# Performance work log

Hardware: AMD Instinct MI355X
Metric: run time of the kernel (lower is better)

## Reference

```python
import jax, jax.numpy as jnp
from jax import lax
import numpy as np

B, L, E, K, NCLS = 128, 1024, 8, 3, 5


def conv1d(x, w, b):
    # x: [N,C,L], w: [O,I,3], padding=1 -> same length
    y = lax.conv_general_dilated(x, w, (1,), [(1, 1)], dimension_numbers=('NCH', 'OIH', 'NCH'))
    return y + b[None, :, None]


def maxpool2(x):
    # MaxPool1d(kernel=2, stride=2), floor mode (VALID drops odd tail)
    return lax.reduce_window(x, -jnp.inf, lax.max, (1, 1, 2), (1, 1, 2), 'VALID')


def setup_inputs():
    key = jax.random.key(0)
    ks = jax.random.split(key, 32)
    s = 0.05
    g = lambda i, shp: jax.random.normal(ks[i], shp, jnp.float32) * s
    inp = {}
    inp['x'] = jax.random.normal(ks[0], (B, 1, L), jnp.float32)
    inp['c1_w'], inp['c1_b'] = g(1, (16, 1, 3)), jnp.zeros((16,), jnp.float32)
    # stacked expert conv params (leading dim = E)
    chans = [(16, 16), (16, 32), (32, 64), (64, 128), (128, 256), (256, 512)]
    for j, (ci, co) in enumerate(chans, start=1):
        inp[f'ew{j}'] = g(1 + j, (E, co, ci, 3))
        inp[f'eb{j}'] = jnp.zeros((E, co), jnp.float32)
    inp['r_w'], inp['r_b'] = g(10, (E, 16)), jnp.zeros((E,), jnp.float32)
    inp['c2_w'], inp['c2_b'] = g(11, (1024, 512, 3)), jnp.zeros((1024,), jnp.float32)
    fl = (L // 8 // 2) * 1024
    inp['f1_w'], inp['f1_b'] = g(12, (256, fl)) * 0.2, jnp.zeros((256,), jnp.float32)
    inp['f2_w'], inp['f2_b'] = g(13, (NCLS, 256)), jnp.zeros((NCLS,), jnp.float32)
    return inp


def reference(x, c1_w, c1_b, ew1, eb1, ew2, eb2, ew3, eb3, ew4, eb4, ew5, eb5, ew6, eb6,
              r_w, r_b, c2_w, c2_b, f1_w, f1_b, f2_w, f2_b):
    b = x.shape[0]
    h = jax.nn.relu(conv1d(x, c1_w, c1_b))            # [B,16,L]
    pooled = h.mean(axis=-1)                           # AdaptiveAvgPool1d(1) -> [B,16]
    # (router noise skipped: eval-mode determinism)
    rlogits = pooled @ r_w.T + r_b                     # [B,E]
    probs = jax.nn.softmax(rlogits, axis=-1)
    tg, ti = lax.top_k(probs, K)                       # [B,K]
    tg = tg / tg.sum(axis=-1, keepdims=True)
    gates = jnp.zeros((b, E), probs.dtype).at[jnp.arange(b)[:, None], ti].set(tg)  # dense [B,E]

    def expert(w1, b1, w2, b2, w3, b3, w4, b4, w5, b5, w6, b6):
        y = conv1d(h, w1, b1)
        y = maxpool2(jax.nn.relu(conv1d(y, w2, b2)))   # block1 -> [B,32,L/2]
        y = conv1d(y, w3, b3)
        y = maxpool2(jax.nn.relu(conv1d(y, w4, b4)))   # block2 -> [B,128,L/4]
        y = conv1d(y, w5, b5)
        y = maxpool2(jax.nn.relu(conv1d(y, w6, b6)))   # block3 -> [B,512,L/8]
        return y

    eouts = jax.vmap(expert)(ew1, eb1, ew2, eb2, ew3, eb3, ew4, eb4, ew5, eb5, ew6, eb6)  # [E,B,512,L/8]
    combined = jnp.einsum('be,ebcl->bcl', gates, eouts)  # gated scatter-combine (zero gate == not dispatched)

    y = maxpool2(jax.nn.relu(conv1d(combined, c2_w, c2_b)))  # [B,1024,L/16]
    y = y.reshape(b, -1)
    y = jax.nn.relu(y @ f1_w.T + f1_b)                 # dropout p=0.05 is identity in eval
    out = y @ f2_w.T + f2_b                            # [B,NCLS]

    mean_probs = probs.mean(axis=0)
    cv = jnp.std(mean_probs, ddof=1) / (mean_probs.mean() + 1e-10)  # torch std is unbiased
    return out, cv ** 2
```

## Files before the change

kernel.cpp:

```cpp
#include <hip/hip_runtime.h>
#include <hip/hip_bf16.h>
#include <math.h>

#define B_   128
#define L_   1024
#define E_   8
#define K_   3

typedef float f32x4 __attribute__((ext_vector_type(4)));
typedef short s8v  __attribute__((ext_vector_type(8)));
typedef unsigned short u16x8 __attribute__((ext_vector_type(8)));

__device__ inline ushort f2bf(float v) {
  union { float f; unsigned u; } x; x.f = v;
  unsigned r = (x.u + 0x7fffu + ((x.u >> 16) & 1u)) >> 16;
  return (ushort)r;
}
__device__ inline float bf2f(ushort h) {
  union { unsigned u; float f; } x; x.u = ((unsigned)h) << 16;
  return x.f;
}

__device__ __forceinline__ void gload_lds16(const ushort* g, ushort* l) {
  __builtin_amdgcn_global_load_lds(
      (const __attribute__((address_space(1))) unsigned int*)g,
      (__attribute__((address_space(3))) unsigned int*)l, 16, 0, 0);
}

__global__ __launch_bounds__(256) void conv1_k(
    const float* __restrict__ x, const float* __restrict__ w,
    const float* __restrict__ bias, float* __restrict__ h,
    float* __restrict__ pooled)
{
  const int b = blockIdx.x;
  const int t = threadIdx.x;
  __shared__ float xs[1026];
  __shared__ float wsm[48];
  __shared__ float bs[16];
  __shared__ float red[4][16];

  for (int i = t; i < 1024; i += 256) xs[i + 1] = x[(size_t)b * 1024 + i];
  if (t == 0) { xs[0] = 0.f; xs[1025] = 0.f; }
  if (t < 48) wsm[t] = w[t];
  if (t < 16) bs[t] = bias[t];
  __syncthreads();

  float ps[16];
#pragma unroll
  for (int c = 0; c < 16; ++c) ps[c] = 0.f;

  for (int li = 0; li < 4; ++li) {
    const int l = t + li * 256;
    const float xm = xs[l], x0 = xs[l + 1], xp = xs[l + 2];
#pragma unroll
    for (int co = 0; co < 16; ++co) {
      float v = fmaf(wsm[co * 3 + 0], xm,
                fmaf(wsm[co * 3 + 1], x0,
                fmaf(wsm[co * 3 + 2], xp, bs[co])));
      v = fmaxf(v, 0.f);
      h[((size_t)b * 16 + co) * 1024 + l] = v;
      ps[co] += v;
    }
  }
#pragma unroll
  for (int co = 0; co < 16; ++co) {
    float v = ps[co];
    for (int off = 32; off > 0; off >>= 1) v += __shfl_down(v, off, 64);
    ps[co] = v;
  }
  const int wid = t >> 6, lane = t & 63;
  if (lane == 0) {
#pragma unroll
    for (int co = 0; co < 16; ++co) red[wid][co] = ps[co];
  }
  __syncthreads();
  if (t < 16) pooled[(size_t)b * 16 + t] =
      (red[0][t] + red[1][t] + red[2][t] + red[3][t]) * (1.f / 1024.f);
}

__global__ void router_k(const float* __restrict__ pooled,
                         const float* __restrict__ rw,
                         const float* __restrict__ rb,
                         float* __restrict__ pair_g, int* __restrict__ pair_e,
                         float* __restrict__ cv2_out)
{
  const int b = threadIdx.x;
  __shared__ float pl[128][8];
  __shared__ float mp[8];

  float pv[16];
#pragma unroll
  for (int i = 0; i < 16; ++i) pv[i] = pooled[(size_t)b * 16 + i];

  float lg[8];
#pragma unroll
  for (int e = 0; e < 8; ++e) {
    float s = rb[e];
#pragma unroll
    for (int i = 0; i < 16; ++i) s = fmaf(pv[i], rw[e * 16 + i], s);
    lg[e] = s;
  }
  float mx = lg[0];
#pragma unroll
  for (int e = 1; e < 8; ++e) mx = fmaxf(mx, lg[e]);
  float pr[8]; float sum = 0.f;
#pragma unroll
  for (int e = 0; e < 8; ++e) { pr[e] = expf(lg[e] - mx); sum += pr[e]; }
  const float inv = 1.f / sum;
#pragma unroll
  for (int e = 0; e < 8; ++e) { pr[e] *= inv; pl[b][e] = pr[e]; }

  bool used[8] = {false,false,false,false,false,false,false,false};
  float tg[3]; int ti[3];
  for (int k = 0; k < 3; ++k) {
    float best = -1.f; int bi = 0;
#pragma unroll
    for (int e = 0; e < 8; ++e)
      if (!used[e] && pr[e] > best) { best = pr[e]; bi = e; }
    used[bi] = true; tg[k] = best; ti[k] = bi;
  }
  const float ts = 1.f / (tg[0] + tg[1] + tg[2]);
  for (int k = 0; k < 3; ++k) {
    pair_g[b * 3 + k] = tg[k] * ts;
    pair_e[b * 3 + k] = ti[k];
  }
  __syncthreads();
  if (b < 8) {
    float s = 0.f;
    for (int i = 0; i < 128; ++i) s += pl[i][b];
    mp[b] = s * (1.f / 128.f);
  }
  __syncthreads();
  if (b == 0) {
    float m = 0.f;
    for (int e = 0; e < 8; ++e) m += mp[e];
    m *= (1.f / 8.f);
    float v = 0.f;
    for (int e = 0; e < 8; ++e) { float d = mp[e] - m; v += d * d; }
    v *= (1.f / 7.f);
    const float cv = sqrtf(v) / (m + 1e-10f);
    cv2_out[0] = cv * cv;
  }
}

template <int CI, int CO, int LIN, bool POOL, int CIC, int CO_T, int CO_R,
          int IN_DIV>
__global__ __launch_bounds__(256) void convR_k(
    const float* __restrict__ in, const float* __restrict__ w,
    const float* __restrict__ bias, float* __restrict__ out,
    const int* __restrict__ pe)
{
  constexpr int CQ  = CO_T / CO_R;
  constexpr int LQ  = 256 / CQ;
  constexpr int L_T = LQ * 4;
  constexpr int LOUT = POOL ? (LIN / 2) : LIN;
  constexpr int RS  = L_T + 8;
  constexpr int CG  = CO_R / 4;

  const int p  = blockIdx.x;
  const int cb = blockIdx.y * CO_T;
  const int l0 = blockIdx.z * L_T;
  const int e  = pe ? pe[p] : 0;
  const float* inp = in + (size_t)(p / IN_DIV) * CI * LIN;
  const float* wp  = w + (size_t)e * CO * CI * 3;

  __shared__ float in_s[CIC * RS];
  __shared__ float w_s[CIC * 3 * CO_T];

  const int t  = threadIdx.x;
  const int cq = t / LQ;
  const int lq = t % LQ;

  float acc[CO_R][4];
#pragma unroll
  for (int c = 0; c < CO_R; ++c)
#pragma unroll
    for (int l = 0; l < 4; ++l) acc[c][l] = 0.f;

  for (int c0 = 0; c0 < CI; c0 += CIC) {
    for (int idx = t; idx < CIC * (L_T + 2); idx += 256) {
      const int ci = idx / (L_T + 2);
      const int j  = idx - ci * (L_T + 2);
      const int gl = l0 + j - 1;
      in_s[ci * RS + j] =
          (gl >= 0 && gl < LIN) ? inp[(size_t)(c0 + ci) * LIN + gl] : 0.f;
    }
    for (int i = t; i < CIC * CO_T; i += 256) {
      const int co = i % CO_T;
      const int ci = i / CO_T;
      const float* wsrc = wp + ((size_t)(cb + co) * CI + (c0 + ci)) * 3;
      const float w0 = wsrc[0], w1 = wsrc[1], w2 = wsrc[2];
      w_s[(ci * 3 + 0) * CO_T + co] = w0;
      w_s[(ci * 3 + 1) * CO_T + co] = w1;
      w_s[(ci * 3 + 2) * CO_T + co] = w2;
    }
    __syncthreads();
#pragma unroll 4
    for (int ci = 0; ci < CIC; ++ci) {
      const float* row = &in_s[ci * RS + lq * 4];
      const float4 xa = *reinterpret_cast<const float4*>(row);
      const float2 xb = *reinterpret_cast<const float2*>(row + 4);
      const float xv[6] = {xa.x, xa.y, xa.z, xa.w, xb.x, xb.y};
      const float* wrow = &w_s[ci * 3 * CO_T + cq * CO_R];
#pragma unroll
      for (int k = 0; k < 3; ++k) {
#pragma unroll
        for (int cg = 0; cg < CG; ++cg) {
          const float4 wv =
              *reinterpret_cast<const float4*>(&wrow[k * CO_T + cg * 4]);
          const float wq[4] = {wv.x, wv.y, wv.z, wv.w};
#pragma unroll
          for (int c = 0; c < 4; ++c)
#pragma unroll
            for (int l = 0; l < 4; ++l)
              acc[cg * 4 + c][l] = fmaf(wq[c], xv[l + k], acc[cg * 4 + c][l]);
        }
      }
    }
    __syncthreads();
  }

#pragma unroll
  for (int c = 0; c < CO_R; ++c) {
    const int co = cb + cq * CO_R + c;
    const float bv = bias[(size_t)e * CO + co];
    const float v0 = acc[c][0] + bv, v1 = acc[c][1] + bv;
    const float v2 = acc[c][2] + bv, v3 = acc[c][3] + bv;
    float* op = out + ((size_t)p * CO + co) * LOUT;
    if (POOL) {
      const int lo = (l0 >> 1) + lq * 2;
      float2 r;
      r.x = fmaxf(fmaxf(v0, v1), 0.f);
      r.y = fmaxf(fmaxf(v2, v3), 0.f);
      *reinterpret_cast<float2*>(&op[lo]) = r;
    } else {
      const int l = l0 + lq * 4;
      *reinterpret_cast<float4*>(&op[l]) = make_float4(v0, v1, v2, v3);
    }
  }
}

__global__ void wprep_k(const float* __restrict__ w, ushort* __restrict__ oh,
                        ushort* __restrict__ ol, int E, int CO, int CI,
                        int total)
{
  const int idx = blockIdx.x * 256 + threadIdx.x;
  if (idx >= total) return;
  const int KC = CI >> 5;
  const int j = idx & 31;
  int r = idx >> 5;
  const int co = r % CO; r /= CO;
  const int kc = r % KC; r /= KC;
  const int tp = r % 3;
  const int e  = r / 3;
  const float v = w[(((size_t)e * CO + co) * CI + (kc * 32 + j)) * 3 + tp];
  const ushort hi = f2bf(v);
  oh[idx] = hi;
  ol[idx] = f2bf(v - bf2f(hi));
}

__global__ __launch_bounds__(256) void t0_k(const float* __restrict__ in,
                                            ushort* __restrict__ oh,
                                            ushort* __restrict__ ol)
{
  __shared__ float tile[32][33];
  const int p  = blockIdx.x;
  const int l0 = blockIdx.y * 32;
  const int tx = threadIdx.x & 31;
  const int ty = threadIdx.x >> 5;

#pragma unroll
  for (int i = 0; i < 4; ++i) {
    const int ci = ty + i * 8;
    tile[ci][tx] = in[(size_t)p * 16384 + (size_t)ci * 512 + l0 + tx];
  }
  __syncthreads();
#pragma unroll
  for (int i = 0; i < 4; ++i) {
    const int l = l0 + ty + i * 8;
    const float v = tile[tx][ty + i * 8];
    const size_t o = ((size_t)p * 514 + 1 + l) * 32 + tx;
    const ushort hi = f2bf(v);
    oh[o] = hi;
    ol[o] = f2bf(v - bf2f(hi));
  }
  if (blockIdx.y == 0 && threadIdx.x < 32) {
    const size_t o0 = (size_t)p * 514 * 32 + threadIdx.x;
    const size_t o1 = ((size_t)p * 514 + 513) * 32 + threadIdx.x;
    oh[o0] = 0; ol[o0] = 0; oh[o1] = 0; ol[o1] = 0;
  }
}

template <int CI, int CO, int L, int OMODE>
__global__ __launch_bounds__(256) void convM_k(
    const ushort* __restrict__ xh, const ushort* __restrict__ xl,
    const ushort* __restrict__ wh, const ushort* __restrict__ wl,
    const float* __restrict__ bias,
    ushort* __restrict__ oh, ushort* __restrict__ ol,
    float* __restrict__ of,
    const int* __restrict__ pe, const float* __restrict__ pg,
    int pair0)
{
  constexpr int KC = CI / 32;
  constexpr int NK = (OMODE == 1) ? 3 : 1;
  const int bx = blockIdx.x;
  const int cb = blockIdx.y * 64;
  const int lz = blockIdx.z * 128;

  __shared__ ushort xs[2][130][32];
  __shared__ ushort wsm[2][3][64][32];
  ushort* xsf = &xs[0][0][0];
  ushort* wsf = &wsm[0][0][0][0];

  const int t = threadIdx.x;
  const int lane = t & 63;
  const int wv = t >> 6;
  const int l16 = lane & 15;
  const int kb8 = (lane >> 4) * 8;

  float gacc[2][4][2];
  if (OMODE == 1) {
#pragma unroll
    for (int a = 0; a < 2; ++a)
#pragma unroll
      for (int b = 0; b < 4; ++b) { gacc[a][b][0] = 0.f; gacc[a][b][1] = 0.f; }
  }

  f32x4 acc[2][4];
  int e = 0; float gate = 1.f; int lp = bx;
  float bv[4];

  for (int kp = 0; kp < NK; ++kp) {
    if (OMODE == 1) {
      const int gp = (pair0 + bx) * 3 + kp;
      e = pe[gp]; gate = pg[gp]; lp = bx * 3 + kp;
    } else if (OMODE == 2) { lp = bx; e = 0; }
    else { lp = bx; e = pe[pair0 + bx]; }

#pragma unroll
    for (int a = 0; a < 2; ++a)
#pragma unroll
      for (int b = 0; b < 4; ++b) acc[a][b] = (f32x4){0.f, 0.f, 0.f, 0.f};

    const size_t xbase = ((size_t)lp * (L + 2) + lz) * CI;

    for (int kc = 0; kc < KC; ++kc) {
      const int c0 = kc * 32;
#pragma unroll
      for (int it = 0; it < 5; ++it) {
        const int g = it * 256 + t;
        if (g < 1040) {
          const int pl = g >= 520;
          const int r = g - pl * 520;
          const int row = r >> 2;
          const int c16 = r & 3;
          const ushort* src =
              (pl ? xl : xh) + xbase + (size_t)row * CI + c0 + c16 * 8;
          gload_lds16(src, xsf + (size_t)g * 8);
        }
      }
#pragma unroll
      for (int it = 0; it < 6; ++it) {
        const int g = it * 256 + t;
        const int pl = g >= 768;
        const int r = g - pl * 768;
        const int tp = r >> 8;
        const int rr = r & 255;
        const int co = rr >> 2;
        const int c16 = rr & 3;
        const ushort* src = (pl ? wl : wh) +
            ((((size_t)e * 3 + tp) * KC + kc) * CO + cb + co) * 32 + c16 * 8;
        gload_lds16(src, wsf + (size_t)g * 8);
      }
      __syncthreads();

      __builtin_amdgcn_s_setprio(1);
#pragma unroll
      for (int tp = 0; tp < 3; ++tp) {
        const int ar = wv * 32 + l16 + tp;
        s8v a00 = *reinterpret_cast<const s8v*>(&xs[0][ar][kb8]);
        s8v a01 = *reinterpret_cast<const s8v*>(&xs[0][ar + 16][kb8]);
        s8v a10 = *reinterpret_cast<const s8v*>(&xs[1][ar][kb8]);
        s8v a11 = *reinterpret_cast<const s8v*>(&xs[1][ar + 16][kb8]);
#pragma unroll
        for (int cs = 0; cs < 4; ++cs) {
          const int brow = cs * 16 + l16;
          s8v bh = *reinterpret_cast<const s8v*>(&wsm[0][tp][brow][kb8]);
          s8v bl = *reinterpret_cast<const s8v*>(&wsm[1][tp][brow][kb8]);
          acc[0][cs] = __builtin_amdgcn_mfma_f32_16x16x32_bf16(a00, bh, acc[0][cs], 0, 0, 0);
          acc[0][cs] = __builtin_amdgcn_mfma_f32_16x16x32_bf16(a00, bl, acc[0][cs], 0, 0, 0);
          acc[0][cs] = __builtin_amdgcn_mfma_f32_16x16x32_bf16(a10, bh, acc[0][cs], 0, 0, 0);
          acc[1][cs] = __builtin_amdgcn_mfma_f32_16x16x32_bf16(a01, bh, acc[1][cs], 0, 0, 0);
          acc[1][cs] = __builtin_amdgcn_mfma_f32_16x16x32_bf16(a01, bl, acc[1][cs], 0, 0, 0);
          acc[1][cs] = __builtin_amdgcn_mfma_f32_16x16x32_bf16(a11, bh, acc[1][cs], 0, 0, 0);
        }
      }
      __builtin_amdgcn_s_setprio(0);
      __syncthreads();
    }

#pragma unroll
    for (int cs = 0; cs < 4; ++cs)
      bv[cs] = bias[(size_t)e * CO + cb + cs * 16 + l16];

    if (OMODE == 1) {
#pragma unroll
      for (int ls = 0; ls < 2; ++ls)
#pragma unroll
        for (int cs = 0; cs < 4; ++cs)
#pragma unroll
          for (int q = 0; q < 2; ++q) {
            const float v0 = acc[ls][cs][q * 2] + bv[cs];
            const float v1 = acc[ls][cs][q * 2 + 1] + bv[cs];
            const float m = fmaxf(fmaxf(v0, v1), 0.f);
            gacc[ls][cs][q] += gate * m;
          }
    }
  }

  if (OMODE == 0) {
#pragma unroll
    for (int ls = 0; ls < 2; ++ls)
#pragma unroll
      for (int cs = 0; cs < 4; ++cs)
#pragma unroll
        for (int r = 0; r < 4; ++r) {
          const int l = lz + wv * 32 + ls * 16 + (lane >> 4) * 4 + r;
          const float v = acc[ls][cs][r] + bv[cs];
          const size_t o = ((size_t)lp * (L + 2) + 1 + l) * CO + cb + cs * 16 + l16;
          const ushort hi = f2bf(v);
          oh[o] = hi;
          ol[o] = f2bf(v - bf2f(hi));
        }
    if (blockIdx.z == 0 && t < 64) {
      const size_t o0 = (size_t)lp * (L + 2) * CO + cb + t;
      const size_t o1 = ((size_t)lp * (L + 2) + (L + 1)) * CO + cb + t;
      oh[o0] = 0; ol[o0] = 0; oh[o1] = 0; ol[o1] = 0;
    }
  } else if (OMODE == 3) {
#pragma unroll
    for (int ls = 0; ls < 2; ++ls)
#pragma unroll
      for (int cs = 0; cs < 4; ++cs)
#pragma unroll
        for (int r = 0; r < 4; r += 2) {
          const float v0 = acc[ls][cs][r] + bv[cs];
          const float v1 = acc[ls][cs][r + 1] + bv[cs];
          const float m = fmaxf(fmaxf(v0, v1), 0.f);
          const int lpp = (lz + wv * 32 + ls * 16 + (lane >> 4) * 4 + r) >> 1;
          const size_t o = ((size_t)lp * (L / 2 + 2) + 1 + lpp) * CO + cb + cs * 16 + l16;
          const ushort hi = f2bf(m);
          oh[o] = hi;
          ol[o] = f2bf(m - bf2f(hi));
        }
    if (blockIdx.z == 0 && t < 64) {
      const size_t o0 = (size_t)lp * (L / 2 + 2) * CO + cb + t;
      const size_t o1 = ((size_t)lp * (L / 2 + 2) + (L / 2 + 1)) * CO + cb + t;
      oh[o0] = 0; ol[o0] = 0; oh[o1] = 0; ol[o1] = 0;
    }
  } else if (OMODE == 1) {
#pragma unroll
    for (int ls = 0; ls < 2; ++ls)
#pragma unroll
      for (int cs = 0; cs < 4; ++cs)
#pragma unroll
        for (int q = 0; q < 2; ++q) {
          const int lpp = (lz + wv * 32 + ls * 16 + (lane >> 4) * 4 + q * 2) >> 1;
          const int co = cb + cs * 16 + l16;
          const size_t o =
              ((size_t)(pair0 + bx) * (L / 2 + 2) + 1 + lpp) * CO + co;
          const float g = gacc[ls][cs][q];
          const ushort hi = f2bf(g);
          oh[o] = hi;
          ol[o] = f2bf(g - bf2f(hi));
        }
    if (blockIdx.z == 0 && t < 64) {
      const size_t o0 = (size_t)(pair0 + bx) * (L / 2 + 2) * CO + cb + t;
      const size_t o1 =
          ((size_t)(pair0 + bx) * (L / 2 + 2) + (L / 2 + 1)) * CO + cb + t;
      oh[o0] = 0; ol[o0] = 0; oh[o1] = 0; ol[o1] = 0;
    }
  } else {
#pragma unroll
    for (int ls = 0; ls < 2; ++ls)
#pragma unroll
      for (int cs = 0; cs < 4; ++cs)
#pragma unroll
        for (int r = 0; r < 4; r += 2) {
          const float v0 = acc[ls][cs][r] + bv[cs];
          const float v1 = acc[ls][cs][r + 1] + bv[cs];
          const float m = fmaxf(fmaxf(v0, v1), 0.f);
          const int lpp = (lz + wv * 32 + ls * 16 + (lane >> 4) * 4 + r) >> 1;
          const int co = cb + cs * 16 + l16;
          const size_t o = ((size_t)lp * CO + co) * (L / 2) + lpp;
          of[o] = m;
        }
  }
}

__global__ __launch_bounds__(256) void fc1M_k(const float* __restrict__ X,
                                              const float* __restrict__ W,
                                              float* __restrict__ part)
{
  __shared__ ushort xs[2][128][32];
  __shared__ ushort wsm[2][64][32];
  const int t = threadIdx.x;
  const int lane = t & 63;
  const int wv = t >> 6;
  const int l16 = lane & 15;
  const int kb8 = (lane >> 4) * 8;
  const int ot = blockIdx.x * 64;
  const size_t k0g = (size_t)blockIdx.y * 512;

  f32x4 acc[2][4];
#pragma unroll
  for (int a = 0; a < 2; ++a)
#pragma unroll
    for (int b = 0; b < 4; ++b) acc[a][b] = (f32x4){0.f, 0.f, 0.f, 0.f};

  const int xrow = t >> 1;
  const int xcol = (t & 1) * 16;
  const int wco  = t >> 2;
  const int wk   = (t & 3) * 8;

  for (int it = 0; it < 16; ++it) {
    const size_t k0 = k0g + it * 32;
    {
      const float* src = X + (size_t)xrow * 65536 + k0 + xcol;
      float v[16];
#pragma unroll
      for (int q = 0; q < 4; ++q)
        *reinterpret_cast<float4*>(&v[q * 4]) =
            *reinterpret_cast<const float4*>(src + q * 4);
#pragma unroll
      for (int q = 0; q < 2; ++q) {
        u16x8 hv, lv;
#pragma unroll
        for (int j = 0; j < 8; ++j) {
          const float f = v[q * 8 + j];
          const ushort h = f2bf(f);
          hv[j] = h;
          lv[j] = f2bf(f - bf2f(h));
        }
        *reinterpret_cast<u16x8*>(&xs[0][xrow][xcol + q * 8]) = hv;
        *reinterpret_cast<u16x8*>(&xs[1][xrow][xcol + q * 8]) = lv;
      }
    }
    {
      const float* src = W + (size_t)(ot + wco) * 65536 + k0 + wk;
      float v[8];
      *reinterpret_cast<float4*>(&v[0]) = *reinterpret_cast<const float4*>(src);
      *reinterpret_cast<float4*>(&v[4]) = *reinterpret_cast<const float4*>(src + 4);
      u16x8 hv, lv;
#pragma unroll
      for (int j = 0; j < 8; ++j) {
        const ushort h = f2bf(v[j]);
        hv[j] = h;
        lv[j] = f2bf(v[j] - bf2f(h));
      }
      *reinterpret_cast<u16x8*>(&wsm[0][wco][wk]) = hv;
      *reinterpret_cast<u16x8*>(&wsm[1][wco][wk]) = lv;
    }
    __syncthreads();
    __builtin_amdgcn_s_setprio(1);
#pragma unroll
    for (int ms = 0; ms < 2; ++ms) {
      const int ar = wv * 32 + ms * 16 + l16;
      s8v ah = *reinterpret_cast<const s8v*>(&xs[0][ar][kb8]);
      s8v al = *reinterpret_cast<const s8v*>(&xs[1][ar][kb8]);
#pragma unroll
      for (int cs = 0; cs < 4; ++cs) {
        const int brow = cs * 16 + l16;
        s8v bh = *reinterpret_cast<const s8v*>(&wsm[0][brow][kb8]);
        s8v bl = *reinterpret_cast<const s8v*>(&wsm[1][brow][kb8]);
        acc[ms][cs] = __builtin_amdgcn_mfma_f32_16x16x32_bf16(ah, bh, acc[ms][cs], 0, 0, 0);
        acc[ms][cs] = __builtin_amdgcn_mfma_f32_16x16x32_bf16(ah, bl, acc[ms][cs], 0, 0, 0);
        acc[ms][cs] = __builtin_amdgcn_mfma_f32_16x16x32_bf16(al, bh, acc[ms][cs], 0, 0, 0);
      }
    }
    __builtin_amdgcn_s_setprio(0);
    __syncthreads();
  }

#pragma unroll
  for (int ms = 0; ms < 2; ++ms)
#pragma unroll
    for (int cs = 0; cs < 4; ++cs)
#pragma unroll
      for (int r = 0; r < 4; ++r) {
        const int row = wv * 32 + ms * 16 + (lane >> 4) * 4 + r;
        const int col = ot + cs * 16 + l16;
        part[((size_t)blockIdx.y * 128 + row) * 256 + col] = acc[ms][cs][r];
      }
}

__global__ void fc1red_k(const float* __restrict__ part,
                         const float* __restrict__ b1, float* __restrict__ o1)
{
  const int idx = blockIdx.x * 256 + threadIdx.x;
  if (idx < 32768) {
    float s = 0.f;
#pragma unroll 8
    for (int z = 0; z < 128; ++z) s += part[(size_t)z * 32768 + idx];
    o1[idx] = fmaxf(s + b1[idx & 255], 0.f);
  }
}

__global__ void fc2_k(const float* __restrict__ o1, const float* __restrict__ w2,
                      const float* __restrict__ b2, float* __restrict__ out)
{
  const int b = blockIdx.x;
  const int lane = threadIdx.x;
  float acc[5] = {0.f, 0.f, 0.f, 0.f, 0.f};
  for (int i = lane; i < 256; i += 64) {
    const float xv = o1[(size_t)b * 256 + i];
#pragma unroll
    for (int o = 0; o < 5; ++o) acc[o] = fmaf(xv, w2[o * 256 + i], acc[o]);
  }
#pragma unroll
  for (int o = 0; o < 5; ++o) {
    for (int off = 32; off > 0; off >>= 1)
      acc[o] += __shfl_down(acc[o], off, 64);
  }
  if (lane == 0) {
#pragma unroll
    for (int o = 0; o < 5; ++o) out[b * 5 + o] = acc[o] + b2[o];
  }
}

extern "C" void kernel_launch(void* const* d_in, const int* in_sizes, int n_in,
                              void* d_out, int out_size, void* d_ws,
                              size_t ws_size, hipStream_t stream)
{
  const float* x   = (const float*)d_in[0];
  const float* c1w = (const float*)d_in[1];
  const float* c1b = (const float*)d_in[2];
  const float* ew[6];
  const float* eb[6];
  for (int j = 0; j < 6; ++j) {
    ew[j] = (const float*)d_in[3 + 2 * j];
    eb[j] = (const float*)d_in[4 + 2 * j];
  }
  const float* rw  = (const float*)d_in[15];
  const float* rb  = (const float*)d_in[16];
  const float* c2w = (const float*)d_in[17];
  const float* c2b = (const float*)d_in[18];
  const float* f1w = (const float*)d_in[19];
  const float* f1b = (const float*)d_in[20];
  const float* f2w = (const float*)d_in[21];
  const float* f2b = (const float*)d_in[22];
  float* out = (float*)d_out;

  const int chunkB = 32;
  const int chunkP = chunkB * 3;
  const int nchunk = 128 / chunkB;

  char* basep = (char*)d_ws;
  size_t off = 0;
  auto alloc = [&](size_t bytes) -> void* {
    off = (off + 255) & ~(size_t)255;
    void* r = basep + off;
    off += bytes;
    return r;
  };

  float* h      = (float*)alloc(2097152ull * 4);
  float* pooled = (float*)alloc(2048ull * 4);
  float* pairg  = (float*)alloc(384ull * 4);
  int*   paire  = (int*)  alloc(384ull * 4);
  float* fc1o   = (float*)alloc(32768ull * 4);

  ushort* xtFh  = (ushort*)alloc(8519680ull * 2 * 2);
  ushort* xtFl  = xtFh + 8519680ull;
  float*  part  = (float*)xtFh;

  const size_t slot_base = (off + 255) & ~(size_t)255;
  char* slotA = (char*)alloc((size_t)chunkP * 33024 * 2 * 2);
  char* slotB = (char*)alloc((size_t)chunkP * 66048 * 2 * 2);
  float* comb = (float*)(basep + slot_base);

  float*  bufA  = (float*)slotA;
  ushort* xt3h  = (ushort*)slotA;
  ushort* xt3l  = xt3h + (size_t)chunkP * 16448;
  ushort* xt5h  = (ushort*)slotA;
  ushort* xt5l  = xt5h + (size_t)chunkP * 33024;
  float*  bufB  = (float*)slotB;
  ushort* yE3h  = (ushort*)slotB;
  ushort* yE3l  = yE3h + (size_t)chunkP * 32896;
  ushort* y5h   = (ushort*)slotB;
  ushort* y5l   = y5h + (size_t)chunkP * 66048;

  ushort* wp3h  = (ushort*)alloc(49152ull * 2);
  ushort* wp3l  = (ushort*)alloc(49152ull * 2);
  ushort* wp4h  = (ushort*)alloc(196608ull * 2);
  ushort* wp4l  = (ushort*)alloc(196608ull * 2);
  ushort* wp5h  = (ushort*)alloc(786432ull * 2);
  ushort* wp5l  = (ushort*)alloc(786432ull * 2);
  ushort* wp6h  = (ushort*)alloc(3145728ull * 2);
  ushort* wp6l  = (ushort*)alloc(3145728ull * 2);
  ushort* wpFh  = (ushort*)alloc(1572864ull * 2);
  ushort* wpFl  = (ushort*)alloc(1572864ull * 2);

  conv1_k<<<128, 256, 0, stream>>>(x, c1w, c1b, h, pooled);
  router_k<<<1, 128, 0, stream>>>(pooled, rw, rb, pairg, paire, out + 640);

  wprep_k<<<(49152 + 255) / 256, 256, 0, stream>>>(ew[2], wp3h, wp3l, 8, 64, 32, 49152);
  wprep_k<<<(196608 + 255) / 256, 256, 0, stream>>>(ew[3], wp4h, wp4l, 8, 128, 64, 196608);
  wprep_k<<<(786432 + 255) / 256, 256, 0, stream>>>(ew[4], wp5h, wp5l, 8, 256, 128, 786432);
  wprep_k<<<(3145728 + 255) / 256, 256, 0, stream>>>(ew[5], wp6h, wp6l, 8, 512, 256, 3145728);
  wprep_k<<<(1572864 + 255) / 256, 256, 0, stream>>>(c2w, wpFh, wpFl, 1, 1024, 512, 1572864);

  for (int c = 0; c < nchunk; ++c) {
    const int b0 = c * chunkB;
    const int p0 = c * chunkP;
    convR_k<16, 16, 1024, false, 16, 16, 4, 3>
        <<<dim3(chunkP, 1, 4), 256, 0, stream>>>(
            h + (size_t)b0 * 16 * 1024, ew[0], eb[0], bufA, paire + p0);
    convR_k<16, 32, 1024, true, 16, 32, 8, 1>
        <<<dim3(chunkP, 1, 4), 256, 0, stream>>>(bufA, ew[1], eb[1], bufB,
                                                 paire + p0);
    t0_k<<<dim3(chunkP, 16), 256, 0, stream>>>(bufB, xt3h, xt3l);
    convM_k<32, 64, 512, 0>
        <<<dim3(chunkP, 1, 4), 256, 0, stream>>>(xt3h, xt3l, wp3h, wp3l, eb[2],
                                                 yE3h, yE3l, nullptr, paire,
                                                 nullptr, p0);
    convM_k<64, 128, 512, 3>
        <<<dim3(chunkP, 2, 4), 256, 0, stream>>>(yE3h, yE3l, wp4h, wp4l, eb[3],
                                                 xt5h, xt5l, nullptr, paire,
                                                 nullptr, p0);
    convM_k<128, 256, 256, 0>
        <<<dim3(chunkP, 4, 2), 256, 0, stream>>>(xt5h, xt5l, wp5h, wp5l, eb[4],
                                                 y5h, y5l, nullptr, paire,
                                                 nullptr, p0);
    convM_k<256, 512, 256, 1>
        <<<dim3(chunkB, 8, 2), 256, 0, stream>>>(y5h, y5l, wp6h, wp6l, eb[5],
                                                 xtFh, xtFl, nullptr,
                                                 paire, pairg, b0);
  }

  convM_k<512, 1024, 128, 2>
      <<<dim3(128, 16, 1), 256, 0, stream>>>(xtFh, xtFl, wpFh, wpFl, c2b,
                                             nullptr, nullptr, comb, nullptr,
                                             nullptr, 0);

  fc1M_k<<<dim3(4, 128), 256, 0, stream>>>(comb, f1w, part);
  fc1red_k<<<128, 256, 0, stream>>>(part, f1b, fc1o);
  fc2_k<<<128, 64, 0, stream>>>(fc1o, f2w, f2b, out);
}
```

Measured before the change: 645.3 us.

## Add larger-tile conv kernel with per-wave 64x64 output tiles

Adds a templated convM2_k in which each wave computes a 64x64 output tile (4 length sub-tiles by 4 channel sub-tiles) instead of 32x64, with a configurable wave layout across length and channels. The block tile grows to 256 positions or 128x128, and layers 4-6 plus the final c2 conv now use it with fewer blocks. The original convM_k is reduced to the OMODE 0 path used by layer 3. The goal is more reuse of each LDS fragment per MFMA and less redundant weight/halo loading. The cost is higher register pressure (64 accumulators plus gate accumulators) and fewer blocks, which may lower occupancy.

```diff
diff --git a/kernel.cpp b/kernel.cpp
--- a/kernel.cpp
+++ b/kernel.cpp
@@ -302,7 +302,6 @@
     int pair0)
 {
   constexpr int KC = CI / 32;
-  constexpr int NK = (OMODE == 1) ? 3 : 1;
   const int bx = blockIdx.x;
   const int cb = blockIdx.y * 64;
   const int lz = blockIdx.z * 128;
@@ -318,15 +317,143 @@
   const int l16 = lane & 15;
   const int kb8 = (lane >> 4) * 8;
 
-  float gacc[2][4][2];
+  const int e = pe[pair0 + bx];
+  const int lp = bx;
+
+  f32x4 acc[2][4];
+#pragma unroll
+  for (int a = 0; a < 2; ++a)
+#pragma unroll
+    for (int b = 0; b < 4; ++b) acc[a][b] = (f32x4){0.f, 0.f, 0.f, 0.f};
+
+  const size_t xbase = ((size_t)lp * (L + 2) + lz) * CI;
+
+  for (int kc = 0; kc < KC; ++kc) {
+    const int c0 = kc * 32;
+#pragma unroll
+    for (int it = 0; it < 5; ++it) {
+      const int g = it * 256 + t;
+      if (g < 1040) {
+        const int pl = g >= 520;
+        const int r = g - pl * 520;
+        const int row = r >> 2;
+        const int c16 = r & 3;
+        const ushort* src =
+            (pl ? xl : xh) + xbase + (size_t)row * CI + c0 + c16 * 8;
+        gload_lds16(src, xsf + (size_t)g * 8);
+      }
+    }
+#pragma unroll
+    for (int it = 0; it < 6; ++it) {
+      const int g = it * 256 + t;
+      const int pl = g >= 768;
+      const int r = g - pl * 768;
+      const int tp = r >> 8;
+      const int rr = r & 255;
+      const int co = rr >> 2;
+      const int c16 = rr & 3;
+      const ushort* src = (pl ? wl : wh) +
+          ((((size_t)e * 3 + tp) * KC + kc) * CO + cb + co) * 32 + c16 * 8;
+      gload_lds16(src, wsf + (size_t)g * 8);
+    }
+    __syncthreads();
+
+    __builtin_amdgcn_s_setprio(1);
+#pragma unroll
+    for (int tp = 0; tp < 3; ++tp) {
+      const int ar = wv * 32 + l16 + tp;
+      s8v a00 = *reinterpret_cast<const s8v*>(&xs[0][ar][kb8]);
+      s8v a01 = *reinterpret_cast<const s8v*>(&xs[0][ar + 16][kb8]);
+      s8v a10 = *reinterpret_cast<const s8v*>(&xs[1][ar][kb8]);
+      s8v a11 = *reinterpret_cast<const s8v*>(&xs[1][ar + 16][kb8]);
+#pragma unroll
+      for (int cs = 0; cs < 4; ++cs) {
+        const int brow = cs * 16 + l16;
+        s8v bh = *reinterpret_cast<const s8v*>(&wsm[0][tp][brow][kb8]);
+        s8v bl = *reinterpret_cast<const s8v*>(&wsm[1][tp][brow][kb8]);
+        acc[0][cs] = __builtin_amdgcn_mfma_f32_16x16x32_bf16(a00, bh, acc[0][cs], 0, 0, 0);
+        acc[0][cs] = __builtin_amdgcn_mfma_f32_16x16x32_bf16(a00, bl, acc[0][cs], 0, 0, 0);
+        acc[0][cs] = __builtin_amdgcn_mfma_f32_16x16x32_bf16(a10, bh, acc[0][cs], 0, 0, 0);
+        acc[1][cs] = __builtin_amdgcn_mfma_f32_16x16x32_bf16(a01, bh, acc[1][cs], 0, 0, 0);
+        acc[1][cs] = __builtin_amdgcn_mfma_f32_16x16x32_bf16(a01, bl, acc[1][cs], 0, 0, 0);
+        acc[1][cs] = __builtin_amdgcn_mfma_f32_16x16x32_bf16(a11, bh, acc[1][cs], 0, 0, 0);
+      }
+    }
+    __builtin_amdgcn_s_setprio(0);
+    __syncthreads();
+  }
+
+  float bv[4];
+#pragma unroll
+  for (int cs = 0; cs < 4; ++cs)
+    bv[cs] = bias[(size_t)e * CO + cb + cs * 16 + l16];
+
+#pragma unroll
+  for (int ls = 0; ls < 2; ++ls)
+#pragma unroll
+    for (int cs = 0; cs < 4; ++cs)
+#pragma unroll
+      for (int r = 0; r < 4; ++r) {
+        const int l = lz + wv * 32 + ls * 16 + (lane >> 4) * 4 + r;
+        const float v = acc[ls][cs][r] + bv[cs];
+        const size_t o = ((size_t)lp * (L + 2) + 1 + l) * CO + cb + cs * 16 + l16;
+        const ushort hi = f2bf(v);
+        oh[o] = hi;
+        ol[o] = f2bf(v - bf2f(hi));
+      }
+  if (blockIdx.z == 0 && t < 64) {
+    const size_t o0 = (size_t)lp * (L + 2) * CO + cb + t;
+    const size_t o1 = ((size_t)lp * (L + 2) + (L + 1)) * CO + cb + t;
+    oh[o0] = 0; ol[o0] = 0; oh[o1] = 0; ol[o1] = 0;
+  }
+}
+
+template <int CI, int CO, int L, int OMODE, int WL, int WC>
+__global__ __launch_bounds__(256) void convM2_k(
+    const ushort* __restrict__ xh, const ushort* __restrict__ xl,
+    const ushort* __restrict__ wh, const ushort* __restrict__ wl,
+    const float* __restrict__ bias,
+    ushort* __restrict__ oh, ushort* __restrict__ ol,
+    float* __restrict__ of,
+    const int* __restrict__ pe, const float* __restrict__ pg,
+    int pair0)
+{
+  constexpr int KC = CI / 32;
+  constexpr int NK = (OMODE == 1) ? 3 : 1;
+  constexpr int LT = WL * 64;
+  constexpr int CT = WC * 64;
+  constexpr int XROWS = LT + 2;
+  constexpr int XG = 2 * XROWS * 4;
+  constexpr int WG = 2 * 3 * CT * 4;
+  constexpr int XIT = (XG + 255) / 256;
+  constexpr int WIT = (WG + 255) / 256;
+
+  const int bx = blockIdx.x;
+  const int cb = blockIdx.y * CT;
+  const int lz = blockIdx.z * LT;
+
+  __shared__ ushort xs[2][XROWS][32];
+  __shared__ ushort wsm[2][3][CT][32];
+  ushort* xsf = &xs[0][0][0];
+  ushort* wsf = &wsm[0][0][0][0];
+
+  const int t = threadIdx.x;
+  const int lane = t & 63;
+  const int wv = t >> 6;
+  const int wvl = wv / WC;
+  const int wvc = wv % WC;
+  const int l16 = lane & 15;
+  const int kb8 = (lane >> 4) * 8;
+
+  float gacc[4][4][2];
   if (OMODE == 1) {
 #pragma unroll
-    for (int a = 0; a < 2; ++a)
+    for (int a = 0; a < 4; ++a)
 #pragma unroll
       for (int b = 0; b < 4; ++b) { gacc[a][b][0] = 0.f; gacc[a][b][1] = 0.f; }
   }
 
-  f32x4 acc[2][4];
+  f32x4 acc[4][4];
   int e = 0; float gate = 1.f; int lp = bx;
   float bv[4];
 
@@ -338,7 +465,7 @@
     else { lp = bx; e = pe[pair0 + bx]; }
 
 #pragma unroll
-    for (int a = 0; a < 2; ++a)
+    for (int a = 0; a < 4; ++a)
 #pragma unroll
       for (int b = 0; b < 4; ++b) acc[a][b] = (f32x4){0.f, 0.f, 0.f, 0.f};
 
@@ -347,11 +474,11 @@
     for (int kc = 0; kc < KC; ++kc) {
       const int c0 = kc * 32;
 #pragma unroll
-      for (int it = 0; it < 5; ++it) {
+      for (int it = 0; it < XIT; ++it) {
         const int g = it * 256 + t;
-        if (g < 1040) {
-          const int pl = g >= 520;
-          const int r = g - pl * 520;
+        if (g < XG) {
+          const int pl = g >= XG / 2;
+          const int r = g - pl * (XG / 2);
           const int row = r >> 2;
           const int c16 = r & 3;
           const ushort* src =
@@ -360,12 +487,12 @@
         }
       }
 #pragma unroll
-      for (int it = 0; it < 6; ++it) {
+      for (int it = 0; it < WIT; ++it) {
         const int g = it * 256 + t;
-        const int pl = g >= 768;
-        const int r = g - pl * 768;
-        const int tp = r >> 8;
-        const int rr = r & 255;
+        const int pl = g >= WG / 2;
+        const int r = g - pl * (WG / 2);
+        const int tp = r / (CT * 4);
+        const int rr = r % (CT * 4);
         const int co = rr >> 2;
         const int c16 = rr & 3;
         const ushort* src = (pl ? wl : wh) +
@@ -377,22 +504,24 @@
       __builtin_amdgcn_s_setprio(1);
 #pragma unroll
       for (int tp = 0; tp < 3; ++tp) {
-        const int ar = wv * 32 + l16 + tp;
-        s8v a00 = *reinterpret_cast<const s8v*>(&xs[0][ar][kb8]);
-        s8v a01 = *reinterpret_cast<const s8v*>(&xs[0][ar + 16][kb8]);
-        s8v a10 = *reinterpret_cast<const s8v*>(&xs[1][ar][kb8]);
-        s8v a11 = *reinterpret_cast<const s8v*>(&xs[1][ar + 16][kb8]);
+        s8v a0[4], a1[4];
+#pragma unroll
+        for (int lt = 0; lt < 4; ++lt) {
+          const int row = wvl * 64 + lt * 16 + l16 + tp;
+          a0[lt] = *reinterpret_cast<const s8v*>(&xs[0][row][kb8]);
+          a1[lt] = *reinterpret_cast<const s8v*>(&xs[1][row][kb8]);
+        }
 #pragma unroll
         for (int cs = 0; cs < 4; ++cs) {
-          const int brow = cs * 16 + l16;
+          const int brow = wvc * 64 + cs * 16 + l16;
           s8v bh = *reinterpret_cast<const s8v*>(&wsm[0][tp][brow][kb8]);
           s8v bl = *reinterpret_cast<const s8v*>(&wsm[1][tp][brow][kb8]);
-          acc[0][cs] = __builtin_amdgcn_mfma_f32_16x16x32_bf16(a00, bh, acc[0][cs], 0, 0, 0);
-          acc[0][cs] = __builtin_amdgcn_mfma_f32_16x16x32_bf16(a00, bl, acc[0][cs], 0, 0, 0);
-          acc[0][cs] = __builtin_amdgcn_mfma_f32_16x16x32_bf16(a10, bh, acc[0][cs], 0, 0, 0);
-          acc[1][cs] = __builtin_amdgcn_mfma_f32_16x16x32_bf16(a01, bh, acc[1][cs], 0, 0, 0);
-          acc[1][cs] = __builtin_amdgcn_mfma_f32_16x16x32_bf16(a01, bl, acc[1][cs], 0, 0, 0);
-          acc[1][cs] = __builtin_amdgcn_mfma_f32_16x16x32_bf16(a11, bh, acc[1][cs], 0, 0, 0);
+#pragma unroll
+          for (int lt = 0; lt < 4; ++lt) {
+            acc[lt][cs] = __builtin_amdgcn_mfma_f32_16x16x32_bf16(a0[lt], bh, acc[lt][cs], 0, 0, 0);
+            acc[lt][cs] = __builtin_amdgcn_mfma_f32_16x16x32_bf16(a0[lt], bl, acc[lt][cs], 0, 0, 0);
+            acc[lt][cs] = __builtin_amdgcn_mfma_f32_16x16x32_bf16(a1[lt], bh, acc[lt][cs], 0, 0, 0);
+          }
         }
       }
       __builtin_amdgcn_s_setprio(0);
@@ -401,80 +530,83 @@
 
 #pragma unroll
     for (int cs = 0; cs < 4; ++cs)
-      bv[cs] = bias[(size_t)e * CO + cb + cs * 16 + l16];
+      bv[cs] = bias[(size_t)e * CO + cb + wvc * 64 + cs * 16 + l16];
 
     if (OMODE == 1) {
 #pragma unroll
-      for (int ls = 0; ls < 2; ++ls)
+      for (int lt = 0; lt < 4; ++lt)
 #pragma unroll
         for (int cs = 0; cs < 4; ++cs)
 #pragma unroll
           for (int q = 0; q < 2; ++q) {
-            const float v0 = acc[ls][cs][q * 2] + bv[cs];
-            const float v1 = acc[ls][cs][q * 2 + 1] + bv[cs];
+            const float v0 = acc[lt][cs][q * 2] + bv[cs];
+            const float v1 = acc[lt][cs][q * 2 + 1] + bv[cs];
             const float m = fmaxf(fmaxf(v0, v1), 0.f);
-            gacc[ls][cs][q] += gate * m;
+            gacc[lt][cs][q] += gate * m;
           }
     }
   }
 
   if (OMODE == 0) {
 #pragma unroll
-    for (int ls = 0; ls < 2; ++ls)
+    for (int lt = 0; lt < 4; ++lt)
 #pragma unroll
       for (int cs = 0; cs < 4; ++cs)
 #pragma unroll
         for (int r = 0; r < 4; ++r) {
-          const int l = lz + wv * 32 + ls * 16 + (lane >> 4) * 4 + r;
-          const float v = acc[ls][cs][r] + bv[cs];
-          const size_t o = ((size_t)lp * (L + 2) + 1 + l) * CO + cb + cs * 16 + l16;
+          const int l = lz + wvl * 64 + lt * 16 + (lane >> 4) * 4 + r;
+          const float v = acc[lt][cs][r] + bv[cs];
+          const size_t o =
+              ((size_t)lp * (L + 2) + 1 + l) * CO + cb + wvc * 64 + cs * 16 + l16;
           const ushort hi = f2bf(v);
           oh[o] = hi;
           ol[o] = f2bf(v - bf2f(hi));
         }
-    if (blockIdx.z == 0 && t < 64) {
+    if (blockIdx.z == 0 && t < CT) {
       const size_t o0 = (size_t)lp * (L + 2) * CO + cb + t;
       const size_t o1 = ((size_t)lp * (L + 2) + (L + 1)) * CO + cb + t;
       oh[o0] = 0; ol[o0] = 0; oh[o1] = 0; ol[o1] = 0;
     }
   } else if (OMODE == 3) {
 #pragma unroll
-    for (int ls = 0; ls < 2; ++ls)
+    for (int lt = 0; lt < 4; ++lt)
 #pragma unroll
       for (int cs = 0; cs < 4; ++cs)
 #pragma unroll
         for (int r = 0; r < 4; r += 2) {
-          const float v0 = acc[ls][cs][r] + bv[cs];
-          const float v1 = acc[ls][cs][r + 1] + bv[cs];
+          const float v0 = acc[lt][cs][r] + bv[cs];
+          const float v1 = acc[lt][cs][r + 1] + bv[cs];
           const float m = fmaxf(fmaxf(v0, v1), 0.f);
-          const int lpp = (lz + wv * 32 + ls * 16 + (lane >> 4) * 4 + r) >> 1;
-          const size_t o = ((size_t)lp * (L / 2 + 2) + 1 + lpp) * CO + cb + cs * 16 + l16;
+          const int lpp = (lz + wvl * 64 + lt * 16 + (lane >> 4) * 4 + r) >> 1;
+          const size_t o = ((size_t)lp * (L / 2 + 2) + 1 + lpp) * CO + cb +
+                           wvc * 64 + cs * 16 + l16;
           const ushort hi = f2bf(m);
           oh[o] = hi;
           ol[o] = f2bf(m - bf2f(hi));
         }
-    if (blockIdx.z == 0 && t < 64) {
+    if (blockIdx.z == 0 && t < CT) {
       const size_t o0 = (size_t)lp * (L / 2 + 2) * CO + cb + t;
       const size_t o1 = ((size_t)lp * (L / 2 + 2) + (L / 2 + 1)) * CO + cb + t;
       oh[o0] = 0; ol[o0] = 0; oh[o1] = 0; ol[o1] = 0;
     }
   } else if (OMODE == 1) {
 #pragma unroll
-    for (int ls = 0; ls < 2; ++ls)
+    for (int lt = 0; lt < 4; ++lt)
 #pragma unroll
       for (int cs = 0; cs < 4; ++cs)
 #pragma unroll
         for (int q = 0; q < 2; ++q) {
-          const int lpp = (lz + wv * 32 + ls * 16 + (lane >> 4) * 4 + q * 2) >> 1;
-          const int co = cb + cs * 16 + l16;
+          const int lpp =
+              (lz + wvl * 64 + lt * 16 + (lane >> 4) * 4 + q * 2) >> 1;
+          const int co = cb + wvc * 64 + cs * 16 + l16;
           const size_t o =
               ((size_t)(pair0 + bx) * (L / 2 + 2) + 1 + lpp) * CO + co;
-          const float g = gacc[ls][cs][q];
+          const float g = gacc[lt][cs][q];
           const ushort hi = f2bf(g);
           oh[o] = hi;
           ol[o] = f2bf(g - bf2f(hi));
         }
-    if (blockIdx.z == 0 && t < 64) {
+    if (blockIdx.z == 0 && t < CT) {
       const size_t o0 = (size_t)(pair0 + bx) * (L / 2 + 2) * CO + cb + t;
       const size_t o1 =
           ((size_t)(pair0 + bx) * (L / 2 + 2) + (L / 2 + 1)) * CO + cb + t;
@@ -482,16 +614,16 @@
     }
   } else {
 #pragma unroll
-    for (int ls = 0; ls < 2; ++ls)
+    for (int lt = 0; lt < 4; ++lt)
 #pragma unroll
       for (int cs = 0; cs < 4; ++cs)
 #pragma unroll
         for (int r = 0; r < 4; r += 2) {
-          const float v0 = acc[ls][cs][r] + bv[cs];
-          const float v1 = acc[ls][cs][r + 1] + bv[cs];
+          const float v0 = acc[lt][cs][r] + bv[cs];
+          const float v1 = acc[lt][cs][r + 1] + bv[cs];
           const float m = fmaxf(fmaxf(v0, v1), 0.f);
-          const int lpp = (lz + wv * 32 + ls * 16 + (lane >> 4) * 4 + r) >> 1;
-          const int co = cb + cs * 16 + l16;
+          const int lpp = (lz + wvl * 64 + lt * 16 + (lane >> 4) * 4 + r) >> 1;
+          const int co = cb + wvc * 64 + cs * 16 + l16;
           const size_t o = ((size_t)lp * CO + co) * (L / 2) + lpp;
           of[o] = m;
         }
@@ -724,24 +856,24 @@
         <<<dim3(chunkP, 1, 4), 256, 0, stream>>>(xt3h, xt3l, wp3h, wp3l, eb[2],
                                                  yE3h, yE3l, nullptr, paire,
                                                  nullptr, p0);
-    convM_k<64, 128, 512, 3>
-        <<<dim3(chunkP, 2, 4), 256, 0, stream>>>(yE3h, yE3l, wp4h, wp4l, eb[3],
+    convM2_k<64, 128, 512, 3, 4, 1>
+        <<<dim3(chunkP, 2, 2), 256, 0, stream>>>(yE3h, yE3l, wp4h, wp4l, eb[3],
                                                  xt5h, xt5l, nullptr, paire,
                                                  nullptr, p0);
-    convM_k<128, 256, 256, 0>
-        <<<dim3(chunkP, 4, 2), 256, 0, stream>>>(xt5h, xt5l, wp5h, wp5l, eb[4],
+    convM2_k<128, 256, 256, 0, 4, 1>
+        <<<dim3(chunkP, 4, 1), 256, 0, stream>>>(xt5h, xt5l, wp5h, wp5l, eb[4],
                                                  y5h, y5l, nullptr, paire,
                                                  nullptr, p0);
-    convM_k<256, 512, 256, 1>
-        <<<dim3(chunkB, 8, 2), 256, 0, stream>>>(y5h, y5l, wp6h, wp6l, eb[5],
+    convM2_k<256, 512, 256, 1, 4, 1>
+        <<<dim3(chunkB, 8, 1), 256, 0, stream>>>(y5h, y5l, wp6h, wp6l, eb[5],
                                                  xtFh, xtFl, nullptr,
                                                  paire, pairg, b0);
   }
 
-  convM_k<512, 1024, 128, 2>
-      <<<dim3(128, 16, 1), 256, 0, stream>>>(xtFh, xtFl, wpFh, wpFl, c2b,
-                                             nullptr, nullptr, comb, nullptr,
-                                             nullptr, 0);
+  convM2_k<512, 1024, 128, 2, 2, 2>
+      <<<dim3(128, 8, 1), 256, 0, stream>>>(xtFh, xtFl, wpFh, wpFl, c2b,
+                                            nullptr, nullptr, comb, nullptr,
+                                            nullptr, 0);
 
   fc1M_k<<<dim3(4, 128), 256, 0, stream>>>(comb, f1w, part);
   fc1red_k<<<128, 256, 0, stream>>>(part, f1b, fc1o);
```

New measurement: 750.2 us. +16.3%, slower.
